# Performance work log

Measured on AMD Instinct MI355X. Metric: run time of the kernel, lower is better.

The kernel has to match this reference:

```python
import jax, jax.numpy as jnp
import numpy as np

N_NODES = 100000
D_IN = 128
D_OUT = 128
N_EDGES = 1600000
BN_EPS = 1e-5
LEAKY_SLOPE = 0.01


def setup_inputs() -> dict:
    key = jax.random.key(0)
    ks = jax.random.split(key, 8)
    x = jax.random.normal(ks[0], (N_NODES, D_IN), dtype=jnp.float32)
    edge_index = jax.random.randint(ks[1], (2, N_EDGES), 0, N_NODES, dtype=jnp.int32)
    scale = 1.0 / np.sqrt(D_IN)
    W = jax.random.uniform(ks[2], (D_IN, D_OUT), jnp.float32, -scale, scale)
    b = jax.random.uniform(ks[3], (D_OUT,), jnp.float32, -scale, scale)
    bn_gamma = jnp.ones((D_IN,), jnp.float32)
    bn_beta = jnp.zeros((D_IN,), jnp.float32)
    bn_mean = jax.random.normal(ks[4], (D_IN,), jnp.float32) * 0.01
    bn_var = jax.random.uniform(ks[5], (D_IN,), jnp.float32, 0.5, 1.5)
    rs_W = jax.random.uniform(ks[6], (D_IN, D_OUT), jnp.float32, -scale, scale)
    rs_b = jax.random.uniform(ks[7], (D_OUT,), jnp.float32, -scale, scale)
    return {"x": x, "edge_index": edge_index, "W": W, "b": b,
            "bn_gamma": bn_gamma, "bn_beta": bn_beta,
            "bn_mean": bn_mean, "bn_var": bn_var,
            "rs_W": rs_W, "rs_b": rs_b}


def reference(x, edge_index, W, b, bn_gamma, bn_beta, bn_mean, bn_var, rs_W, rs_b):
    N = x.shape[0]
    # F.normalize: row-wise L2 normalization (eps=1e-12)
    nrm = jnp.sqrt(jnp.sum(x * x, axis=1, keepdims=True))
    x = x / jnp.maximum(nrm, 1e-12)
    # BatchNorm1d (eval mode, running stats)
    x = (x - bn_mean) * jax.lax.rsqrt(bn_var + BN_EPS) * bn_gamma + bn_beta
    # GCNConv: add self-loops, symmetric normalization
    loops = jnp.arange(N, dtype=edge_index.dtype)
    src = jnp.concatenate([edge_index[0], loops])  # [E+N] source j
    dst = jnp.concatenate([edge_index[1], loops])  # [E+N] target i
    deg = jax.ops.segment_sum(jnp.ones(dst.shape, x.dtype), dst, num_segments=N)
    dinv = jax.lax.rsqrt(deg)  # self-loops guarantee deg >= 1
    norm = dinv[src] * dinv[dst]  # [E+N]
    xw = x @ W  # [N, D_OUT]
    msgs = xw[src] * norm[:, None]  # [E+N, D_OUT] gather
    out = jax.ops.segment_sum(msgs, dst, num_segments=N) + b  # scatter-add
    # residual linear on the normalized+BN'd input
    out = out + x @ rs_W + rs_b
    # LeakyReLU (dropout is identity in eval mode)
    return jnp.where(out >= 0, out, LEAKY_SLOPE * out)
```

## Files before the change

### kernel.cpp

```cpp
#include <hip/hip_runtime.h>
#include <hip/hip_fp16.h>


#define NN 100000
#define DD 128
#define EE 1600000
#define BN_EPS 1e-5f
#define SLOPE 0.01f

#define NBKT 98
#define BWID 1024
#define CAPP 20480
#define EPB  4096

struct __align__(8) H4 { __half2 a, b; };

typedef _Float16 f16x8 __attribute__((ext_vector_type(8)));
typedef float    f32x4 __attribute__((ext_vector_type(4)));

__global__ void k_prep(const float* __restrict__ W, const float* __restrict__ rsW,
                       const float* __restrict__ b, const float* __restrict__ rb,
                       __half* __restrict__ WhT, float* __restrict__ bias2,
                       int* __restrict__ gcur) {
  int blk = blockIdx.x, t = threadIdx.x;
  if (blk == 128) {
    if (t < DD) bias2[t] = b[t] + rb[t];
    if (t < NBKT) gcur[t] = t * CAPP;
    return;
  }
  float v = (t < 128) ? W[t * 128 + blk] : rsW[(t - 128) * 128 + blk];
  WhT[blk * 256 + t] = __float2half(v);
}

__global__ __launch_bounds__(256) void k_binA(const int* __restrict__ src,
                                              const int* __restrict__ dst,
                                              int* __restrict__ gcur,
                                              int* __restrict__ pairs) {
  __shared__ int hist[2][NBKT];
  __shared__ int cur[2][NBKT];
  int t = threadIdx.x;
  int w2 = (t >> 6) & 1;
  if (t < NBKT) { hist[0][t] = 0; hist[1][t] = 0; }
  __syncthreads();
  int e0 = blockIdx.x * EPB;
  #pragma unroll 4
  for (int i = 0; i < EPB / 256; ++i) {
    int e = e0 + i * 256 + t;
    if (e < EE) atomicAdd(&hist[w2][dst[e] >> 10], 1);
  }
  __syncthreads();
  if (t < NBKT) {
    int h0 = hist[0][t], h1 = hist[1][t];
    int b0 = atomicAdd(&gcur[t], h0 + h1);
    cur[0][t] = b0;
    cur[1][t] = b0 + h0;
  }
  __syncthreads();
  #pragma unroll 4
  for (int i = 0; i < EPB / 256; ++i) {
    int e = e0 + i * 256 + t;
    if (e < EE) {
      int d = dst[e], s = src[e];
      int bk = d >> 10;
      int r = atomicAdd(&cur[w2][bk], 1);
      pairs[r] = ((d & 1023) << 17) | s;
    }
  }
}

__global__ __launch_bounds__(1024) void k_binB(const int* __restrict__ gcur,
                                               const int* __restrict__ pairs,
                                               int* __restrict__ csr,
                                               int2* __restrict__ startdeg,
                                               float* __restrict__ dinv) {
  __shared__ int hist[BWID];
  __shared__ int excl[BWID];
  __shared__ int wsum[16];
  int b = blockIdx.x, t = threadIdx.x;
  hist[t] = 0;
  __syncthreads();
  int pbase = b * CAPP;
  int cnt = gcur[b] - pbase;
  for (int i = t; i < cnt; i += BWID)
    atomicAdd(&hist[pairs[pbase + i] >> 17], 1);
  __syncthreads();
  int v = hist[t];
  int lane = t & 63, w = t >> 6;
  int incl = v;
  #pragma unroll
  for (int off = 1; off < 64; off <<= 1) {
    int n = __shfl_up(incl, off, 64);
    if (lane >= off) incl += n;
  }
  if (lane == 63) wsum[w] = incl;
  __syncthreads();
  if (t < 16) {
    int orig = wsum[t];
    int s = orig;
    #pragma unroll
    for (int off = 1; off < 16; off <<= 1) {
      int n = __shfl_up(s, off, 64);
      if (t >= off) s += n;
    }
    wsum[t] = s - orig;
  }
  __syncthreads();
  int myexcl = (incl - v) + wsum[w];
  excl[t] = myexcl;
  int node = b * BWID + t;
  if (node < NN) {
    dinv[node] = rsqrtf((float)(v + 1));
    startdeg[node] = make_int2(pbase + myexcl, v);
  }
  __syncthreads();
  for (int i = t; i < cnt; i += BWID) {
    int p = pairs[pbase + i];
    int pos = atomicAdd(&excl[p >> 17], 1);
    csr[pbase + pos] = p & 0x1FFFF;
  }
}

__global__ void k_norm_bn(const float* __restrict__ x,
                          const float* __restrict__ gamma,
                          const float* __restrict__ beta,
                          const float* __restrict__ mean,
                          const float* __restrict__ var,
                          const float* __restrict__ dinv,
                          __half* __restrict__ Ah, __half* __restrict__ zp) {
  int row = blockIdx.x * 4 + (threadIdx.x >> 6);
  int lane = threadIdx.x & 63;
  if (row >= NN) return;
  float2 v = ((const float2*)(x + (size_t)row * DD))[lane];
  float ss = v.x * v.x + v.y * v.y;
  #pragma unroll
  for (int off = 32; off > 0; off >>= 1) ss += __shfl_xor(ss, off);
  float s = 1.0f / fmaxf(sqrtf(ss), 1e-12f);
  float di = dinv[row];
  int c = lane * 2;
  float g0 = gamma[c]     * rsqrtf(var[c]     + BN_EPS);
  float g1 = gamma[c + 1] * rsqrtf(var[c + 1] + BN_EPS);
  float ox = (v.x * s - mean[c])     * g0 + beta[c];
  float oy = (v.y * s - mean[c + 1]) * g1 + beta[c + 1];
  ((__half2*)(Ah + (size_t)row * 256 + 128))[lane] = __floats2half2_rn(ox, oy);
  ((__half2*)(zp + (size_t)row * DD))[lane] = __floats2half2_rn(di * ox, di * oy);
}

__global__ void k_aggregate(const __half* __restrict__ zp,
                            __half* __restrict__ Ah,
                            const int2* __restrict__ startdeg,
                            const int* __restrict__ csr,
                            const float* __restrict__ dinv) {
  int node = blockIdx.x * 4 + (threadIdx.x >> 6);
  int lane = threadIdx.x & 63;
  int half = lane >> 5;
  int l32  = lane & 31;
  int2 sd = startdeg[node];
  int beg = sd.x, end = sd.x + sd.y;
  float di = dinv[node];
  const H4* zr = (const H4*)zp;
  float4 acc = make_float4(0.f, 0.f, 0.f, 0.f);
  int k = beg + half;
  for (; k + 6 < end; k += 8) {
    int j0 = csr[k], j1 = csr[k + 2], j2 = csr[k + 4], j3 = csr[k + 6];
    H4 a0 = zr[(size_t)j0 * 32 + l32];
    H4 a1 = zr[(size_t)j1 * 32 + l32];
    H4 a2 = zr[(size_t)j2 * 32 + l32];
    H4 a3 = zr[(size_t)j3 * 32 + l32];
    float2 f0a = __half22float2(a0.a), f0b = __half22float2(a0.b);
    float2 f1a = __half22float2(a1.a), f1b = __half22float2(a1.b);
    float2 f2a = __half22float2(a2.a), f2b = __half22float2(a2.b);
    float2 f3a = __half22float2(a3.a), f3b = __half22float2(a3.b);
    acc.x += (f0a.x + f1a.x) + (f2a.x + f3a.x);
    acc.y += (f0a.y + f1a.y) + (f2a.y + f3a.y);
    acc.z += (f0b.x + f1b.x) + (f2b.x + f3b.x);
    acc.w += (f0b.y + f1b.y) + (f2b.y + f3b.y);
  }
  for (; k < end; k += 2) {
    int j0 = csr[k];
    H4 a0 = zr[(size_t)j0 * 32 + l32];
    float2 fa = __half22float2(a0.a), fb = __half22float2(a0.b);
    acc.x += fa.x; acc.y += fa.y; acc.z += fb.x; acc.w += fb.y;
  }
  acc.x += __shfl_xor(acc.x, 32, 64);
  acc.y += __shfl_xor(acc.y, 32, 64);
  acc.z += __shfl_xor(acc.z, 32, 64);
  acc.w += __shfl_xor(acc.w, 32, 64);
  if (half == 0) {
    H4 zs = zr[(size_t)node * 32 + l32];
    float2 za = __half22float2(zs.a), zb2 = __half22float2(zs.b);
    H4 o;
    o.a = __floats2half2_rn((acc.x + za.x) * di, (acc.y + za.y) * di);
    o.b = __floats2half2_rn((acc.z + zb2.x) * di, (acc.w + zb2.y) * di);
    ((H4*)Ah)[(size_t)node * 64 + l32] = o;
  }
}

__global__ __launch_bounds__(512, 2) void k_gemm(
    const __half* __restrict__ Ah, const __half* __restrict__ WhT,
    const float* __restrict__ bias2, float* __restrict__ out) {
  __shared__ __align__(16) char Bs[65536];
  const int tid = threadIdx.x;
  const int w  = tid >> 6;
  const int l  = tid & 63;
  const int lm = l & 15;
  const int lk = l >> 4;
  const int row0 = blockIdx.x * 256 + w * 32;

  int rA0 = row0 + lm;
  int rA1 = row0 + 16 + lm;
  if (rA0 >= NN) rA0 = NN - 1;
  if (rA1 >= NN) rA1 = NN - 1;

  const __half* a0p = Ah + (size_t)rA0 * 256 + lk * 8;
  const __half* a1p = Ah + (size_t)rA1 * 256 + lk * 8;
  f16x8 a0[8], a1[8];
  #pragma unroll
  for (int ks = 0; ks < 8; ++ks) {
    a0[ks] = *(const f16x8*)(a0p + ks * 32);
    a1[ks] = *(const f16x8*)(a1p + ks * 32);
  }

  #pragma unroll
  for (int i = 0; i < 8; ++i) {
    int idx = tid + i * 512;
    int byte = idx * 16;
    int swz = byte ^ (((byte >> 9) & 7) << 4);
    *(float4*)(Bs + swz) = ((const float4*)WhT)[idx];
  }
  __syncthreads();

  f32x4 acc0[8], acc1[8];
  #pragma unroll
  for (int c = 0; c < 8; ++c) {
    acc0[c] = (f32x4)(0.f);
    acc1[c] = (f32x4)(0.f);
  }

  #pragma unroll
  for (int ks = 0; ks < 8; ++ks) {
    #pragma unroll
    for (int c = 0; c < 8; ++c) {
      int byte = (c * 16 + lm) * 512 + lk * 16 + ks * 64;
      f16x8 b = *(const f16x8*)(Bs + (byte ^ ((lm & 7) << 4)));
      acc0[c] = __builtin_amdgcn_mfma_f32_16x16x32_f16(a0[ks], b, acc0[c], 0, 0, 0);
      acc1[c] = __builtin_amdgcn_mfma_f32_16x16x32_f16(a1[ks], b, acc1[c], 0, 0, 0);
    }
  }

  int orow0 = row0 + lk * 4;
  int orow1 = row0 + 16 + lk * 4;
  #pragma unroll
  for (int c = 0; c < 8; ++c) {
    int col = c * 16 + lm;
    float bs = bias2[col];
    #pragma unroll
    for (int r = 0; r < 4; ++r) {
      int g0 = orow0 + r;
      if (g0 < NN) {
        float v = acc0[c][r] + bs;
        out[(size_t)g0 * 128 + col] = (v >= 0.f) ? v : SLOPE * v;
      }
      int g1 = orow1 + r;
      if (g1 < NN) {
        float v = acc1[c][r] + bs;
        out[(size_t)g1 * 128 + col] = (v >= 0.f) ? v : SLOPE * v;
      }
    }
  }
}

extern "C" void kernel_launch(void* const* d_in, const int* in_sizes, int n_in,
                              void* d_out, int out_size, void* d_ws, size_t ws_size,
                              hipStream_t stream) {
  const float* x     = (const float*)d_in[0];
  const int*   ei    = (const int*)d_in[1];
  const float* W     = (const float*)d_in[2];
  const float* b     = (const float*)d_in[3];
  const float* gamma = (const float*)d_in[4];
  const float* beta  = (const float*)d_in[5];
  const float* mean  = (const float*)d_in[6];
  const float* var   = (const float*)d_in[7];
  const float* rsW   = (const float*)d_in[8];
  const float* rsb   = (const float*)d_in[9];
  float* out = (float*)d_out;
  const int* src = ei;
  const int* dst = ei + EE;

  __half* Ah       = (__half*)d_ws;
  __half* zp       = Ah + (size_t)NN * 256;
  int2*   startdeg = (int2*)(zp + (size_t)NN * DD);
  float*  dinv     = (float*)(startdeg + NN);
  int*    gcur     = (int*)(dinv + NN);
  int*    pairs    = gcur + 128;
  int*    csr      = pairs + NBKT * CAPP;
  __half* WhT      = (__half*)(csr + NBKT * CAPP);
  float*  bias2    = (float*)(WhT + 128 * 256);

  k_prep<<<129, 256, 0, stream>>>(W, rsW, b, rsb, WhT, bias2, gcur);
  k_binA<<<(EE + EPB - 1) / EPB, 256, 0, stream>>>(src, dst, gcur, pairs);
  k_binB<<<NBKT, 1024, 0, stream>>>(gcur, pairs, csr, startdeg, dinv);
  k_norm_bn<<<NN / 4, 256, 0, stream>>>(x, gamma, beta, mean, var, dinv, Ah, zp);
  k_aggregate<<<NN / 4, 256, 0, stream>>>(zp, Ah, startdeg, csr, dinv);
  k_gemm<<<(NN + 255) / 256, 512, 0, stream>>>(Ah, WhT, bias2, out);
}
```

Before: 281.0 us.

## Fold weight prep into binning kernel and map one half-wave per node in aggregation

The separate prep kernel is removed. Weight transpose and bias sum now run in extra blocks of the binning kernel, and the bucket cursors are zeroed with a memset, so bucket offsets become relative. The aggregation kernel now gives each 32-lane half-wave its own node instead of splitting a node's edges across two halves. It loads 8 neighbor indices and rows at a time and drops the cross-half shuffle reduction. The aim is to cut one launch and raise memory-level parallelism in the gather, at the cost of less balanced work between the two halves of a wave on high-degree nodes.

```diff
diff --git a/kernel.cpp b/kernel.cpp
--- a/kernel.cpp
+++ b/kernel.cpp
@@ -12,33 +12,36 @@
 #define BWID 1024
 #define CAPP 20480
 #define EPB  4096
+#define EBLK 391
 
 struct __align__(8) H4 { __half2 a, b; };
 
 typedef _Float16 f16x8 __attribute__((ext_vector_type(8)));
 typedef float    f32x4 __attribute__((ext_vector_type(4)));
-
-__global__ void k_prep(const float* __restrict__ W, const float* __restrict__ rsW,
-                       const float* __restrict__ b, const float* __restrict__ rb,
-                       __half* __restrict__ WhT, float* __restrict__ bias2,
-                       int* __restrict__ gcur) {
-  int blk = blockIdx.x, t = threadIdx.x;
-  if (blk == 128) {
-    if (t < DD) bias2[t] = b[t] + rb[t];
-    if (t < NBKT) gcur[t] = t * CAPP;
-    return;
-  }
-  float v = (t < 128) ? W[t * 128 + blk] : rsW[(t - 128) * 128 + blk];
-  WhT[blk * 256 + t] = __float2half(v);
-}
 
 __global__ __launch_bounds__(256) void k_binA(const int* __restrict__ src,
                                               const int* __restrict__ dst,
                                               int* __restrict__ gcur,
-                                              int* __restrict__ pairs) {
+                                              int* __restrict__ pairs,
+                                              const float* __restrict__ W,
+                                              const float* __restrict__ rsW,
+                                              const float* __restrict__ b,
+                                              const float* __restrict__ rb,
+                                              __half* __restrict__ WhT,
+                                              float* __restrict__ bias2) {
+  int t = threadIdx.x;
+  if (blockIdx.x >= EBLK) {
+    int blk = blockIdx.x - EBLK;
+    if (blk == 128) {
+      if (t < DD) bias2[t] = b[t] + rb[t];
+    } else {
+      float v = (t < 128) ? W[t * 128 + blk] : rsW[(t - 128) * 128 + blk];
+      WhT[blk * 256 + t] = __float2half(v);
+    }
+    return;
+  }
   __shared__ int hist[2][NBKT];
   __shared__ int cur[2][NBKT];
-  int t = threadIdx.x;
   int w2 = (t >> 6) & 1;
   if (t < NBKT) { hist[0][t] = 0; hist[1][t] = 0; }
   __syncthreads();
@@ -63,7 +66,7 @@
       int d = dst[e], s = src[e];
       int bk = d >> 10;
       int r = atomicAdd(&cur[w2][bk], 1);
-      pairs[r] = ((d & 1023) << 17) | s;
+      pairs[(size_t)bk * CAPP + r] = ((d & 1023) << 17) | s;
     }
   }
 }
@@ -80,7 +83,7 @@
   hist[t] = 0;
   __syncthreads();
   int pbase = b * CAPP;
-  int cnt = gcur[b] - pbase;
+  int cnt = gcur[b];
   for (int i = t; i < cnt; i += BWID)
     atomicAdd(&hist[pairs[pbase + i] >> 17], 1);
   __syncthreads();
@@ -150,49 +153,54 @@
                             const int2* __restrict__ startdeg,
                             const int* __restrict__ csr,
                             const float* __restrict__ dinv) {
-  int node = blockIdx.x * 4 + (threadIdx.x >> 6);
   int lane = threadIdx.x & 63;
   int half = lane >> 5;
   int l32  = lane & 31;
+  int node = blockIdx.x * 8 + (threadIdx.x >> 6) * 2 + half;
   int2 sd = startdeg[node];
-  int beg = sd.x, end = sd.x + sd.y;
+  int k = sd.x, end = sd.x + sd.y;
   float di = dinv[node];
   const H4* zr = (const H4*)zp;
   float4 acc = make_float4(0.f, 0.f, 0.f, 0.f);
-  int k = beg + half;
-  for (; k + 6 < end; k += 8) {
-    int j0 = csr[k], j1 = csr[k + 2], j2 = csr[k + 4], j3 = csr[k + 6];
-    H4 a0 = zr[(size_t)j0 * 32 + l32];
-    H4 a1 = zr[(size_t)j1 * 32 + l32];
-    H4 a2 = zr[(size_t)j2 * 32 + l32];
-    H4 a3 = zr[(size_t)j3 * 32 + l32];
-    float2 f0a = __half22float2(a0.a), f0b = __half22float2(a0.b);
-    float2 f1a = __half22float2(a1.a), f1b = __half22float2(a1.b);
-    float2 f2a = __half22float2(a2.a), f2b = __half22float2(a2.b);
-    float2 f3a = __half22float2(a3.a), f3b = __half22float2(a3.b);
-    acc.x += (f0a.x + f1a.x) + (f2a.x + f3a.x);
-    acc.y += (f0a.y + f1a.y) + (f2a.y + f3a.y);
-    acc.z += (f0b.x + f1b.x) + (f2b.x + f3b.x);
-    acc.w += (f0b.y + f1b.y) + (f2b.y + f3b.y);
-  }
-  for (; k < end; k += 2) {
+  for (; k + 8 <= end; k += 8) {
+    int j[8];
+    #pragma unroll
+    for (int u = 0; u < 8; ++u) j[u] = csr[k + u];
+    H4 a[8];
+    #pragma unroll
+    for (int u = 0; u < 8; ++u) a[u] = zr[(size_t)j[u] * 32 + l32];
+    #pragma unroll
+    for (int u = 0; u < 8; ++u) {
+      float2 fa = __half22float2(a[u].a), fb = __half22float2(a[u].b);
+      acc.x += fa.x; acc.y += fa.y; acc.z += fb.x; acc.w += fb.y;
+    }
+  }
+  if (k + 4 <= end) {
+    int j[4];
+    #pragma unroll
+    for (int u = 0; u < 4; ++u) j[u] = csr[k + u];
+    H4 a[4];
+    #pragma unroll
+    for (int u = 0; u < 4; ++u) a[u] = zr[(size_t)j[u] * 32 + l32];
+    #pragma unroll
+    for (int u = 0; u < 4; ++u) {
+      float2 fa = __half22float2(a[u].a), fb = __half22float2(a[u].b);
+      acc.x += fa.x; acc.y += fa.y; acc.z += fb.x; acc.w += fb.y;
+    }
+    k += 4;
+  }
+  for (; k < end; ++k) {
     int j0 = csr[k];
     H4 a0 = zr[(size_t)j0 * 32 + l32];
     float2 fa = __half22float2(a0.a), fb = __half22float2(a0.b);
     acc.x += fa.x; acc.y += fa.y; acc.z += fb.x; acc.w += fb.y;
   }
-  acc.x += __shfl_xor(acc.x, 32, 64);
-  acc.y += __shfl_xor(acc.y, 32, 64);
-  acc.z += __shfl_xor(acc.z, 32, 64);
-  acc.w += __shfl_xor(acc.w, 32, 64);
-  if (half == 0) {
-    H4 zs = zr[(size_t)node * 32 + l32];
-    float2 za = __half22float2(zs.a), zb2 = __half22float2(zs.b);
-    H4 o;
-    o.a = __floats2half2_rn((acc.x + za.x) * di, (acc.y + za.y) * di);
-    o.b = __floats2half2_rn((acc.z + zb2.x) * di, (acc.w + zb2.y) * di);
-    ((H4*)Ah)[(size_t)node * 64 + l32] = o;
-  }
+  H4 zs = zr[(size_t)node * 32 + l32];
+  float2 za = __half22float2(zs.a), zb2 = __half22float2(zs.b);
+  H4 o;
+  o.a = __floats2half2_rn((acc.x + za.x) * di, (acc.y + za.y) * di);
+  o.b = __floats2half2_rn((acc.z + zb2.x) * di, (acc.w + zb2.y) * di);
+  ((H4*)Ah)[(size_t)node * 64 + l32] = o;
 }
 
 __global__ __launch_bounds__(512, 2) void k_gemm(
@@ -296,10 +304,11 @@
   __half* WhT      = (__half*)(csr + NBKT * CAPP);
   float*  bias2    = (float*)(WhT + 128 * 256);
 
-  k_prep<<<129, 256, 0, stream>>>(W, rsW, b, rsb, WhT, bias2, gcur);
-  k_binA<<<(EE + EPB - 1) / EPB, 256, 0, stream>>>(src, dst, gcur, pairs);
+  hipMemsetAsync(gcur, 0, 128 * sizeof(int), stream);
+  k_binA<<<EBLK + 129, 256, 0, stream>>>(src, dst, gcur, pairs,
+                                         W, rsW, b, rsb, WhT, bias2);
   k_binB<<<NBKT, 1024, 0, stream>>>(gcur, pairs, csr, startdeg, dinv);
   k_norm_bn<<<NN / 4, 256, 0, stream>>>(x, gamma, beta, mean, var, dinv, Ah, zp);
-  k_aggregate<<<NN / 4, 256, 0, stream>>>(zp, Ah, startdeg, csr, dinv);
+  k_aggregate<<<NN / 8, 256, 0, stream>>>(zp, Ah, startdeg, csr, dinv);
   k_gemm<<<(NN + 255) / 256, 512, 0, stream>>>(Ah, WhT, bias2, out);
 }
```

Result: faster. 272.6 us (-3.0%).
